# Optimization experiments

Measured on AMD Instinct MI355X. Metric: run time of the kernel, lower is better.

The kernel has to match this reference:

```python
import jax, jax.numpy as jnp
import numpy as np

N, E = 50000, 800000
NIN, H, C = 128, 4, 32          # per-head dim C = nout // nhead
ED = 44                          # edge_dim = (nin-16)/4 + 16
HC = H * C


def setup_inputs() -> dict:
    key = jax.random.key(0)
    ks = jax.random.split(key, 12)
    s = 0.05
    return {
        "x": jax.random.normal(ks[0], (N, NIN), jnp.float32),
        "edge_index": jax.random.randint(ks[1], (2, E), 0, N, jnp.int64),
        "edge_attr": jax.random.normal(ks[2], (E, ED), jnp.float32),
        "Wq": jax.random.normal(ks[3], (NIN, HC), jnp.float32) * s,
        "bq": jnp.zeros((HC,), jnp.float32),
        "Wk": jax.random.normal(ks[4], (NIN, HC), jnp.float32) * s,
        "bk": jnp.zeros((HC,), jnp.float32),
        "Wv": jax.random.normal(ks[5], (NIN, HC), jnp.float32) * s,
        "bv": jnp.zeros((HC,), jnp.float32),
        "We": jax.random.normal(ks[6], (ED, HC), jnp.float32) * s,  # lin_edge has no bias in PyG
        "Wskip": jax.random.normal(ks[7], (NIN, HC), jnp.float32) * s,
        "bskip": jnp.zeros((HC,), jnp.float32),
    }


def reference(x, edge_index, edge_attr, Wq, bq, Wk, bk, Wv, bv, We, Wskip, bskip):
    src, dst = edge_index[0], edge_index[1]  # messages flow src -> dst
    q = (x @ Wq + bq).reshape(N, H, C)
    k = (x @ Wk + bk).reshape(N, H, C)
    v = (x @ Wv + bv).reshape(N, H, C)
    e = (edge_attr @ We).reshape(E, H, C)

    k_j = k[src] + e                         # [E, H, C]
    v_j = v[src] + e                         # [E, H, C]
    alpha = jnp.einsum('ehc,ehc->eh', q[dst], k_j) / jnp.sqrt(jnp.float32(C))

    # segment softmax over incoming edges of each destination node
    m = jax.ops.segment_max(alpha, dst, num_segments=N)          # [N, H]
    a = jnp.exp(alpha - m[dst])
    denom = jax.ops.segment_sum(a, dst, num_segments=N)          # [N, H]
    a = a / (denom[dst] + 1e-16)

    agg = jax.ops.segment_sum(v_j * a[:, :, None], dst, num_segments=N)  # [N, H, C]
    out = agg.reshape(N, HC) + (x @ Wskip + bskip)               # concat heads + root skip
    return out
```

## Files before the change

### kernel.cpp

```cpp
#include <hip/hip_runtime.h>

#define N_      50000
#define E_      800000
#define HC_     128
#define ED_     44
#define NH_     4
#define DEGCAP_ 96

__global__ __launch_bounds__(256) void k_lin(
    const float* __restrict__ x,
    const float* __restrict__ Wq, const float* __restrict__ bq,
    const float* __restrict__ Wk, const float* __restrict__ bk,
    const float* __restrict__ Wv, const float* __restrict__ bv,
    const float* __restrict__ Wsk, const float* __restrict__ bsk,
    float* __restrict__ q, float* __restrict__ k, float* __restrict__ v,
    float* __restrict__ skip)
{
    __shared__ float xs[32 * 128];
    const int n0 = blockIdx.x * 32;
    const int t  = threadIdx.x;

    #pragma unroll
    for (int i = 0; i < 4; ++i) {
        int idx = t + i * 256;
        int row = idx >> 5;
        float4 a = make_float4(0.f, 0.f, 0.f, 0.f);
        if (n0 + row < N_) a = ((const float4*)x)[(size_t)n0 * 32 + idx];
        *(float4*)&xs[idx * 4] = a;
    }
    __syncthreads();

    const float* Wm[4] = {Wq, Wk, Wv, Wsk};
    const float* bm[4] = {bq, bk, bv, bsk};
    float* om[4] = {q, k, v, skip};
    const int mat = blockIdx.y;
    const float* W = Wm[mat];

    const int tx = t & 31, ty = t >> 5;
    float acc[4][4];
    #pragma unroll
    for (int r = 0; r < 4; ++r) {
        acc[r][0] = 0.f; acc[r][1] = 0.f; acc[r][2] = 0.f; acc[r][3] = 0.f;
    }

    float4 wb[4];
    #pragma unroll
    for (int dd = 0; dd < 4; ++dd)
        wb[dd] = *(const float4*)(W + dd * 128 + tx * 4);

    for (int s = 0; s < 32; ++s) {
        int sn = (s + 1) & 31;
        float4 wn[4];
        #pragma unroll
        for (int dd = 0; dd < 4; ++dd)
            wn[dd] = *(const float4*)(W + (sn * 4 + dd) * 128 + tx * 4);
        #pragma unroll
        for (int r = 0; r < 4; ++r) {
            float4 xv = *(const float4*)&xs[(ty * 4 + r) * 128 + s * 4];
            acc[r][0] += xv.x * wb[0].x + xv.y * wb[1].x + xv.z * wb[2].x + xv.w * wb[3].x;
            acc[r][1] += xv.x * wb[0].y + xv.y * wb[1].y + xv.z * wb[2].y + xv.w * wb[3].y;
            acc[r][2] += xv.x * wb[0].z + xv.y * wb[1].z + xv.z * wb[2].z + xv.w * wb[3].z;
            acc[r][3] += xv.x * wb[0].w + xv.y * wb[1].w + xv.z * wb[2].w + xv.w * wb[3].w;
        }
        #pragma unroll
        for (int dd = 0; dd < 4; ++dd) wb[dd] = wn[dd];
    }

    float4 b4 = *(const float4*)(bm[mat] + tx * 4);
    float* o = om[mat];
    #pragma unroll
    for (int r = 0; r < 4; ++r) {
        int n = n0 + ty * 4 + r;
        if (n < N_) {
            float4 rr = make_float4(acc[r][0] + b4.x, acc[r][1] + b4.y,
                                    acc[r][2] + b4.z, acc[r][3] + b4.w);
            ((float4*)(o + (size_t)n * 128))[tx] = rr;
        }
    }
}

__global__ __launch_bounds__(256) void k_scatter(const int* __restrict__ ei,
                                                 int* __restrict__ cnt,
                                                 int2* __restrict__ csr) {
    int e = blockIdx.x * 256 + threadIdx.x;
    int src = ei[e], dst = ei[E_ + e];
    int pos = atomicAdd(&cnt[dst], 1);
    if (pos < DEGCAP_) csr[(size_t)dst * DEGCAP_ + pos] = make_int2(src, e);
}

__global__ __launch_bounds__(256) void k_node(
    const int* __restrict__ cnt, const int2* __restrict__ csr,
    const float* __restrict__ ea, const float* __restrict__ We,
    const float* __restrict__ q, const float* __restrict__ k,
    const float* __restrict__ v, const float* __restrict__ skip,
    float* __restrict__ out)
{
    __shared__ float sq [4][128];
    __shared__ float sqw[4][176];
    __shared__ float srd[4][324];
    const int t = threadIdx.x, w = t >> 6, l = t & 63;
    const int n = blockIdx.x * 4 + w;

    float2 q2 = ((const float2*)(q + (size_t)n * HC_))[l];
    ((float2*)&sq[w][0])[l] = q2;

    {
        const int h = l >> 4, i16 = l & 15;
        const int d0 = 3 * i16;
        const int de0 = (d0     < ED_) ? d0     : ED_ - 1;
        const int de1 = (d0 + 1 < ED_) ? d0 + 1 : ED_ - 1;
        const int de2 = (d0 + 2 < ED_) ? d0 + 2 : ED_ - 1;
        const float* qh  = &sq[w][h * 32];
        const float* w0p = We + de0 * HC_ + h * 32;
        const float* w1p = We + de1 * HC_ + h * 32;
        const float* w2p = We + de2 * HC_ + h * 32;
        float qw0 = 0.f, qw1 = 0.f, qw2 = 0.f;
        #pragma unroll
        for (int i = 0; i < 8; ++i) {
            float4 q4 = *(const float4*)(qh  + i * 4);
            float4 a0 = *(const float4*)(w0p + i * 4);
            float4 a1 = *(const float4*)(w1p + i * 4);
            float4 a2 = *(const float4*)(w2p + i * 4);
            qw0 += q4.x*a0.x + q4.y*a0.y + q4.z*a0.z + q4.w*a0.w;
            qw1 += q4.x*a1.x + q4.y*a1.y + q4.z*a1.z + q4.w*a1.w;
            qw2 += q4.x*a2.x + q4.y*a2.y + q4.z*a2.z + q4.w*a2.w;
        }
        if (d0     < ED_) sqw[w][h * ED_ + d0]     = qw0;
        if (d0 + 1 < ED_) sqw[w][h * ED_ + d0 + 1] = qw1;
        if (d0 + 2 < ED_) sqw[w][h * ED_ + d0 + 2] = qw2;
    }

    const int g = l >> 4, ii = l & 15, eh = ii >> 2, si = ii & 3;
    const float4 qa = *(const float4*)&sq[w][eh * 32 + si * 8];
    const float4 qb = *(const float4*)&sq[w][eh * 32 + si * 8 + 4];
    float4 w0, w1, w2;
    {
        const float* wp = &sqw[w][eh * ED_ + si * 12];
        w0 = *(const float4*)wp;
        w1 = *(const float4*)(wp + 4);
        w2 = (si < 3) ? *(const float4*)(wp + 8) : make_float4(0.f,0.f,0.f,0.f);
    }
    const int eoff2 = (si < 3) ? si * 12 + 8 : 36;

    int deg = cnt[n];
    deg = deg < DEGCAP_ ? deg : DEGCAP_;
    const int2* crow = csr + (size_t)n * DEGCAP_;
    int2 c0 = make_int2(0, 0);
    if (deg > 0) c0 = crow[l < deg ? l : deg - 1];

    float4 av0 = make_float4(0.f,0.f,0.f,0.f), av1 = make_float4(0.f,0.f,0.f,0.f);
    float4 aeA = make_float4(0.f,0.f,0.f,0.f), aeB = make_float4(0.f,0.f,0.f,0.f);
    float4 aeC = make_float4(0.f,0.f,0.f,0.f);
    float ssum = 0.f;

    const int lim = deg < 64 ? deg : 64;
    for (int base = 0; base < lim; base += 8) {
        const int slotA = base + g,     slotB = base + 4 + g;
        const int scA = slotA < lim ? slotA : lim - 1;
        const int scB = slotB < lim ? slotB : lim - 1;
        const int sA = __shfl(c0.x, scA), eEA = __shfl(c0.y, scA);
        const int sB = __shfl(c0.x, scB), eEB = __shfl(c0.y, scB);

        const float* kpA = k + (size_t)sA * HC_ + eh * 32 + si * 8;
        const float* vpA = v + (size_t)sA * HC_ + eh * 32 + si * 8;
        const float* epA = ea + (size_t)eEA * ED_;
        const float* kpB = k + (size_t)sB * HC_ + eh * 32 + si * 8;
        const float* vpB = v + (size_t)sB * HC_ + eh * 32 + si * 8;
        const float* epB = ea + (size_t)eEB * ED_;
        const float4 kaA = *(const float4*)kpA;
        const float4 kbA = *(const float4*)(kpA + 4);
        const float4 vaA = *(const float4*)vpA;
        const float4 vbA = *(const float4*)(vpA + 4);
        const float4 e0A = *(const float4*)(epA + si * 12);
        const float4 e1A = *(const float4*)(epA + si * 12 + 4);
        const float4 e2A = *(const float4*)(epA + eoff2);
        const float4 kaB = *(const float4*)kpB;
        const float4 kbB = *(const float4*)(kpB + 4);
        const float4 vaB = *(const float4*)vpB;
        const float4 vbB = *(const float4*)(vpB + 4);
        const float4 e0B = *(const float4*)(epB + si * 12);
        const float4 e1B = *(const float4*)(epB + si * 12 + 4);
        const float4 e2B = *(const float4*)(epB + eoff2);

        float pA = qa.x*kaA.x + qa.y*kaA.y + qa.z*kaA.z + qa.w*kaA.w
                 + qb.x*kbA.x + qb.y*kbA.y + qb.z*kbA.z + qb.w*kbA.w
                 + w0.x*e0A.x + w0.y*e0A.y + w0.z*e0A.z + w0.w*e0A.w
                 + w1.x*e1A.x + w1.y*e1A.y + w1.z*e1A.z + w1.w*e1A.w
                 + w2.x*e2A.x + w2.y*e2A.y + w2.z*e2A.z + w2.w*e2A.w;
        float pB = qa.x*kaB.x + qa.y*kaB.y + qa.z*kaB.z + qa.w*kaB.w
                 + qb.x*kbB.x + qb.y*kbB.y + qb.z*kbB.z + qb.w*kbB.w
                 + w0.x*e0B.x + w0.y*e0B.y + w0.z*e0B.z + w0.w*e0B.w
                 + w1.x*e1B.x + w1.y*e1B.y + w1.z*e1B.z + w1.w*e1B.w
                 + w2.x*e2B.x + w2.y*e2B.y + w2.z*e2B.z + w2.w*e2B.w;
        pA += __shfl_xor(pA, 1);  pB += __shfl_xor(pB, 1);
        pA += __shfl_xor(pA, 2);  pB += __shfl_xor(pB, 2);
        const float alA = fminf(pA * 0.17677669529663687f, 40.f);
        const float alB = fminf(pB * 0.17677669529663687f, 40.f);
        const float wjA = (slotA < lim) ? __expf(alA) : 0.f;
        const float wjB = (slotB < lim) ? __expf(alB) : 0.f;

        ssum  += wjA + wjB;
        av0.x += wjA * vaA.x + wjB * vaB.x;  av0.y += wjA * vaA.y + wjB * vaB.y;
        av0.z += wjA * vaA.z + wjB * vaB.z;  av0.w += wjA * vaA.w + wjB * vaB.w;
        av1.x += wjA * vbA.x + wjB * vbB.x;  av1.y += wjA * vbA.y + wjB * vbB.y;
        av1.z += wjA * vbA.z + wjB * vbB.z;  av1.w += wjA * vbA.w + wjB * vbB.w;
        aeA.x += wjA * e0A.x + wjB * e0B.x;  aeA.y += wjA * e0A.y + wjB * e0B.y;
        aeA.z += wjA * e0A.z + wjB * e0B.z;  aeA.w += wjA * e0A.w + wjB * e0B.w;
        aeB.x += wjA * e1A.x + wjB * e1B.x;  aeB.y += wjA * e1A.y + wjB * e1B.y;
        aeB.z += wjA * e1A.z + wjB * e1B.z;  aeB.w += wjA * e1A.w + wjB * e1B.w;
        aeC.x += wjA * e2A.x + wjB * e2B.x;  aeC.y += wjA * e2A.y + wjB * e2B.y;
        aeC.z += wjA * e2A.z + wjB * e2B.z;  aeC.w += wjA * e2A.w + wjB * e2B.w;
    }

    for (int j = 64; j < deg; ++j) {
        int2 se = crow[j];
        int sA = __builtin_amdgcn_readfirstlane(se.x);
        int eA = __builtin_amdgcn_readfirstlane(se.y);
        const float* kp = k + (size_t)sA * HC_ + eh * 32 + si * 8;
        const float* vp = v + (size_t)sA * HC_ + eh * 32 + si * 8;
        const float* ep = ea + (size_t)eA * ED_;
        float4 ka = *(const float4*)kp, kb = *(const float4*)(kp + 4);
        float4 va = *(const float4*)vp, vb = *(const float4*)(vp + 4);
        float4 e0 = *(const float4*)(ep + si * 12);
        float4 e1 = *(const float4*)(ep + si * 12 + 4);
        float4 e2 = *(const float4*)(ep + eoff2);
        float p = qa.x*ka.x + qa.y*ka.y + qa.z*ka.z + qa.w*ka.w
                + qb.x*kb.x + qb.y*kb.y + qb.z*kb.z + qb.w*kb.w
                + w0.x*e0.x + w0.y*e0.y + w0.z*e0.z + w0.w*e0.w
                + w1.x*e1.x + w1.y*e1.y + w1.z*e1.z + w1.w*e1.w
                + w2.x*e2.x + w2.y*e2.y + w2.z*e2.z + w2.w*e2.w;
        p += __shfl_xor(p, 1);
        p += __shfl_xor(p, 2);
        float wj = (g == 0) ? __expf(fminf(p * 0.17677669529663687f, 40.f)) : 0.f;
        ssum  += wj;
        av0.x += wj * va.x; av0.y += wj * va.y; av0.z += wj * va.z; av0.w += wj * va.w;
        av1.x += wj * vb.x; av1.y += wj * vb.y; av1.z += wj * vb.z; av1.w += wj * vb.w;
        aeA.x += wj * e0.x; aeA.y += wj * e0.y; aeA.z += wj * e0.z; aeA.w += wj * e0.w;
        aeB.x += wj * e1.x; aeB.y += wj * e1.y; aeB.z += wj * e1.z; aeB.w += wj * e1.w;
        aeC.x += wj * e2.x; aeC.y += wj * e2.y; aeC.z += wj * e2.z; aeC.w += wj * e2.w;
    }

    #pragma unroll
    for (int d = 16; d <= 32; d <<= 1) {
        ssum  += __shfl_xor(ssum,  d);
        av0.x += __shfl_xor(av0.x, d); av0.y += __shfl_xor(av0.y, d);
        av0.z += __shfl_xor(av0.z, d); av0.w += __shfl_xor(av0.w, d);
        av1.x += __shfl_xor(av1.x, d); av1.y += __shfl_xor(av1.y, d);
        av1.z += __shfl_xor(av1.z, d); av1.w += __shfl_xor(av1.w, d);
        aeA.x += __shfl_xor(aeA.x, d); aeA.y += __shfl_xor(aeA.y, d);
        aeA.z += __shfl_xor(aeA.z, d); aeA.w += __shfl_xor(aeA.w, d);
        aeB.x += __shfl_xor(aeB.x, d); aeB.y += __shfl_xor(aeB.y, d);
        aeB.z += __shfl_xor(aeB.z, d); aeB.w += __shfl_xor(aeB.w, d);
        aeC.x += __shfl_xor(aeC.x, d); aeC.y += __shfl_xor(aeC.y, d);
        aeC.z += __shfl_xor(aeC.z, d); aeC.w += __shfl_xor(aeC.w, d);
    }

    float* sav = &srd[w][0];
    float* sae = &srd[w][128];
    float* ssm = &srd[w][320];
    if (g == 0) {
        *(float4*)&sav[eh * 32 + si * 8]     = av0;
        *(float4*)&sav[eh * 32 + si * 8 + 4] = av1;
        *(float4*)&sae[eh * 48 + si * 12]     = aeA;
        *(float4*)&sae[eh * 48 + si * 12 + 4] = aeB;
        if (si < 3) *(float4*)&sae[eh * 48 + si * 12 + 8] = aeC;
        if (si == 0) ssm[eh] = ssum;
    }

    const int h2 = l >> 4;
    float2 acc = *(const float2*)&sav[2 * l];
    float evx = 0.f, evy = 0.f;
    for (int d = 0; d < ED_; ++d) {
        float aw = sae[h2 * 48 + d];
        float2 wd = ((const float2*)(We + d * HC_))[l];
        evx += aw * wd.x;
        evy += aw * wd.y;
    }
    float inv = 1.0f / (ssm[h2] + 1e-16f);
    float2 sk = ((const float2*)(skip + (size_t)n * HC_))[l];
    ((float2*)(out + (size_t)n * HC_))[l] =
        make_float2((acc.x + evx) * inv + sk.x, (acc.y + evy) * inv + sk.y);
}

extern "C" void kernel_launch(void* const* d_in, const int* in_sizes, int n_in,
                              void* d_out, int out_size, void* d_ws, size_t ws_size,
                              hipStream_t stream)
{
    const float* x   = (const float*)d_in[0];
    const int*   ei  = (const int*)d_in[1];
    const float* ea  = (const float*)d_in[2];
    const float* Wq  = (const float*)d_in[3];
    const float* bq  = (const float*)d_in[4];
    const float* Wk  = (const float*)d_in[5];
    const float* bk  = (const float*)d_in[6];
    const float* Wv  = (const float*)d_in[7];
    const float* bv  = (const float*)d_in[8];
    const float* We  = (const float*)d_in[9];
    const float* Wsk = (const float*)d_in[10];
    const float* bsk = (const float*)d_in[11];
    float* out = (float*)d_out;

    float* ws    = (float*)d_ws;
    float* q     = ws;
    float* k     = q     + (size_t)N_ * HC_;
    float* v     = k     + (size_t)N_ * HC_;
    float* skip  = v     + (size_t)N_ * HC_;
    int*   cnt   = (int*)(skip + (size_t)N_ * HC_);
    int2*  csr   = (int2*)(cnt + N_);

    hipMemsetAsync(cnt, 0, N_ * sizeof(int), stream);
    k_lin    <<<dim3((N_ + 31) / 32, 4), 256, 0, stream>>>(
        x, Wq, bq, Wk, bk, Wv, bv, Wsk, bsk, q, k, v, skip);
    k_scatter<<<E_ / 256, 256, 0, stream>>>(ei, cnt, csr);
    k_node   <<<N_ / 4, 256, 0, stream>>>(cnt, csr, ea, We, q, k, v,
                                          skip, out);
}
```

Measured before the change: 702.1 us.

## Split node aggregation into 8-edge chunks with atomic partial accumulation

Instead of one wavefront per destination node walking all incoming edges, a new pass builds a list of (node, chunk) work items of eight edges each, and each wavefront handles one chunk. Partial softmax numerators, weighted edge sums and denominators are atomically added into global buffers, and a separate finalize kernel applies the We projection, normalization and skip. The CSR now stores only edge ids, with the source read from edge_index. This aims to balance load across skewed degrees and raise occupancy. The cost is many global float atomics, an extra zeroed workspace of about 300 floats per node, two more launches, and a q·We recomputation per chunk rather than per node.

```diff
diff --git a/kernel.cpp b/kernel.cpp
--- a/kernel.cpp
+++ b/kernel.cpp
@@ -6,6 +6,8 @@
 #define ED_     44
 #define NH_     4
 #define DEGCAP_ 96
+#define CHK_    8
+#define LCAP_   (E_ / CHK_ + N_)
 
 __global__ __launch_bounds__(256) void k_lin(
     const float* __restrict__ x,
@@ -81,25 +83,42 @@
 
 __global__ __launch_bounds__(256) void k_scatter(const int* __restrict__ ei,
                                                  int* __restrict__ cnt,
-                                                 int2* __restrict__ csr) {
+                                                 int* __restrict__ csr) {
     int e = blockIdx.x * 256 + threadIdx.x;
-    int src = ei[e], dst = ei[E_ + e];
+    int dst = ei[E_ + e];
     int pos = atomicAdd(&cnt[dst], 1);
-    if (pos < DEGCAP_) csr[(size_t)dst * DEGCAP_ + pos] = make_int2(src, e);
-}
-
-__global__ __launch_bounds__(256) void k_node(
-    const int* __restrict__ cnt, const int2* __restrict__ csr,
-    const float* __restrict__ ea, const float* __restrict__ We,
-    const float* __restrict__ q, const float* __restrict__ k,
-    const float* __restrict__ v, const float* __restrict__ skip,
-    float* __restrict__ out)
+    if (pos < DEGCAP_) csr[(size_t)dst * DEGCAP_ + pos] = e;
+}
+
+__global__ __launch_bounds__(256) void k_chunks(const int* __restrict__ cnt,
+                                                int* __restrict__ chcnt,
+                                                int* __restrict__ chlist) {
+    int n = blockIdx.x * 256 + threadIdx.x;
+    if (n >= N_) return;
+    int deg = cnt[n];
+    deg = deg < DEGCAP_ ? deg : DEGCAP_;
+    int nc = (deg + CHK_ - 1) / CHK_;
+    if (nc == 0) return;
+    int pos = atomicAdd(chcnt, nc);
+    for (int j = 0; j < nc; ++j) chlist[pos + j] = (n << 4) | j;
+}
+
+__global__ __launch_bounds__(512) void k_node(
+    const int* __restrict__ chcnt, const int* __restrict__ chlist,
+    const int* __restrict__ cnt, const int* __restrict__ csr,
+    const int* __restrict__ ei, const float* __restrict__ ea,
+    const float* __restrict__ We, const float* __restrict__ q,
+    const float* __restrict__ k, const float* __restrict__ v,
+    float* __restrict__ sav, float* __restrict__ sae,
+    float* __restrict__ sbuf)
 {
-    __shared__ float sq [4][128];
-    __shared__ float sqw[4][176];
-    __shared__ float srd[4][324];
+    __shared__ float sq [8][128];
+    __shared__ float sqw[8][176];
     const int t = threadIdx.x, w = t >> 6, l = t & 63;
-    const int n = blockIdx.x * 4 + w;
+    const int id = blockIdx.x * 8 + w;
+    if (id >= chcnt[0]) return;
+    const int p = chlist[id];
+    const int n = p >> 4, c = p & 15;
 
     float2 q2 = ((const float2*)(q + (size_t)n * HC_))[l];
     ((float2*)&sq[w][0])[l] = q2;
@@ -144,101 +163,67 @@
 
     int deg = cnt[n];
     deg = deg < DEGCAP_ ? deg : DEGCAP_;
-    const int2* crow = csr + (size_t)n * DEGCAP_;
-    int2 c0 = make_int2(0, 0);
-    if (deg > 0) c0 = crow[l < deg ? l : deg - 1];
-
-    float4 av0 = make_float4(0.f,0.f,0.f,0.f), av1 = make_float4(0.f,0.f,0.f,0.f);
-    float4 aeA = make_float4(0.f,0.f,0.f,0.f), aeB = make_float4(0.f,0.f,0.f,0.f);
-    float4 aeC = make_float4(0.f,0.f,0.f,0.f);
-    float ssum = 0.f;
-
-    const int lim = deg < 64 ? deg : 64;
-    for (int base = 0; base < lim; base += 8) {
-        const int slotA = base + g,     slotB = base + 4 + g;
-        const int scA = slotA < lim ? slotA : lim - 1;
-        const int scB = slotB < lim ? slotB : lim - 1;
-        const int sA = __shfl(c0.x, scA), eEA = __shfl(c0.y, scA);
-        const int sB = __shfl(c0.x, scB), eEB = __shfl(c0.y, scB);
-
-        const float* kpA = k + (size_t)sA * HC_ + eh * 32 + si * 8;
-        const float* vpA = v + (size_t)sA * HC_ + eh * 32 + si * 8;
-        const float* epA = ea + (size_t)eEA * ED_;
-        const float* kpB = k + (size_t)sB * HC_ + eh * 32 + si * 8;
-        const float* vpB = v + (size_t)sB * HC_ + eh * 32 + si * 8;
-        const float* epB = ea + (size_t)eEB * ED_;
-        const float4 kaA = *(const float4*)kpA;
-        const float4 kbA = *(const float4*)(kpA + 4);
-        const float4 vaA = *(const float4*)vpA;
-        const float4 vbA = *(const float4*)(vpA + 4);
-        const float4 e0A = *(const float4*)(epA + si * 12);
-        const float4 e1A = *(const float4*)(epA + si * 12 + 4);
-        const float4 e2A = *(const float4*)(epA + eoff2);
-        const float4 kaB = *(const float4*)kpB;
-        const float4 kbB = *(const float4*)(kpB + 4);
-        const float4 vaB = *(const float4*)vpB;
-        const float4 vbB = *(const float4*)(vpB + 4);
-        const float4 e0B = *(const float4*)(epB + si * 12);
-        const float4 e1B = *(const float4*)(epB + si * 12 + 4);
-        const float4 e2B = *(const float4*)(epB + eoff2);
-
-        float pA = qa.x*kaA.x + qa.y*kaA.y + qa.z*kaA.z + qa.w*kaA.w
-                 + qb.x*kbA.x + qb.y*kbA.y + qb.z*kbA.z + qb.w*kbA.w
-                 + w0.x*e0A.x + w0.y*e0A.y + w0.z*e0A.z + w0.w*e0A.w
-                 + w1.x*e1A.x + w1.y*e1A.y + w1.z*e1A.z + w1.w*e1A.w
-                 + w2.x*e2A.x + w2.y*e2A.y + w2.z*e2A.z + w2.w*e2A.w;
-        float pB = qa.x*kaB.x + qa.y*kaB.y + qa.z*kaB.z + qa.w*kaB.w
-                 + qb.x*kbB.x + qb.y*kbB.y + qb.z*kbB.z + qb.w*kbB.w
-                 + w0.x*e0B.x + w0.y*e0B.y + w0.z*e0B.z + w0.w*e0B.w
-                 + w1.x*e1B.x + w1.y*e1B.y + w1.z*e1B.z + w1.w*e1B.w
-                 + w2.x*e2B.x + w2.y*e2B.y + w2.z*e2B.z + w2.w*e2B.w;
-        pA += __shfl_xor(pA, 1);  pB += __shfl_xor(pB, 1);
-        pA += __shfl_xor(pA, 2);  pB += __shfl_xor(pB, 2);
-        const float alA = fminf(pA * 0.17677669529663687f, 40.f);
-        const float alB = fminf(pB * 0.17677669529663687f, 40.f);
-        const float wjA = (slotA < lim) ? __expf(alA) : 0.f;
-        const float wjB = (slotB < lim) ? __expf(alB) : 0.f;
-
-        ssum  += wjA + wjB;
-        av0.x += wjA * vaA.x + wjB * vaB.x;  av0.y += wjA * vaA.y + wjB * vaB.y;
-        av0.z += wjA * vaA.z + wjB * vaB.z;  av0.w += wjA * vaA.w + wjB * vaB.w;
-        av1.x += wjA * vbA.x + wjB * vbB.x;  av1.y += wjA * vbA.y + wjB * vbB.y;
-        av1.z += wjA * vbA.z + wjB * vbB.z;  av1.w += wjA * vbA.w + wjB * vbB.w;
-        aeA.x += wjA * e0A.x + wjB * e0B.x;  aeA.y += wjA * e0A.y + wjB * e0B.y;
-        aeA.z += wjA * e0A.z + wjB * e0B.z;  aeA.w += wjA * e0A.w + wjB * e0B.w;
-        aeB.x += wjA * e1A.x + wjB * e1B.x;  aeB.y += wjA * e1A.y + wjB * e1B.y;
-        aeB.z += wjA * e1A.z + wjB * e1B.z;  aeB.w += wjA * e1A.w + wjB * e1B.w;
-        aeC.x += wjA * e2A.x + wjB * e2B.x;  aeC.y += wjA * e2A.y + wjB * e2B.y;
-        aeC.z += wjA * e2A.z + wjB * e2B.z;  aeC.w += wjA * e2A.w + wjB * e2B.w;
-    }
-
-    for (int j = 64; j < deg; ++j) {
-        int2 se = crow[j];
-        int sA = __builtin_amdgcn_readfirstlane(se.x);
-        int eA = __builtin_amdgcn_readfirstlane(se.y);
-        const float* kp = k + (size_t)sA * HC_ + eh * 32 + si * 8;
-        const float* vp = v + (size_t)sA * HC_ + eh * 32 + si * 8;
-        const float* ep = ea + (size_t)eA * ED_;
-        float4 ka = *(const float4*)kp, kb = *(const float4*)(kp + 4);
-        float4 va = *(const float4*)vp, vb = *(const float4*)(vp + 4);
-        float4 e0 = *(const float4*)(ep + si * 12);
-        float4 e1 = *(const float4*)(ep + si * 12 + 4);
-        float4 e2 = *(const float4*)(ep + eoff2);
-        float p = qa.x*ka.x + qa.y*ka.y + qa.z*ka.z + qa.w*ka.w
-                + qb.x*kb.x + qb.y*kb.y + qb.z*kb.z + qb.w*kb.w
-                + w0.x*e0.x + w0.y*e0.y + w0.z*e0.z + w0.w*e0.w
-                + w1.x*e1.x + w1.y*e1.y + w1.z*e1.z + w1.w*e1.w
-                + w2.x*e2.x + w2.y*e2.y + w2.z*e2.z + w2.w*e2.w;
-        p += __shfl_xor(p, 1);
-        p += __shfl_xor(p, 2);
-        float wj = (g == 0) ? __expf(fminf(p * 0.17677669529663687f, 40.f)) : 0.f;
-        ssum  += wj;
-        av0.x += wj * va.x; av0.y += wj * va.y; av0.z += wj * va.z; av0.w += wj * va.w;
-        av1.x += wj * vb.x; av1.y += wj * vb.y; av1.z += wj * vb.z; av1.w += wj * vb.w;
-        aeA.x += wj * e0.x; aeA.y += wj * e0.y; aeA.z += wj * e0.z; aeA.w += wj * e0.w;
-        aeB.x += wj * e1.x; aeB.y += wj * e1.y; aeB.z += wj * e1.z; aeB.w += wj * e1.w;
-        aeC.x += wj * e2.x; aeC.y += wj * e2.y; aeC.z += wj * e2.z; aeC.w += wj * e2.w;
-    }
+    const int rem = deg - c * CHK_;
+
+    int idx = c * CHK_ + (l & 7);
+    if (idx >= deg) idx = deg - 1;
+    const int eId  = csr[(size_t)n * DEGCAP_ + idx];
+    const int srcN = ei[eId];
+
+    const int slotA = g, slotB = 4 + g;
+    const int sA = __shfl(srcN, slotA), eEA = __shfl(eId, slotA);
+    const int sB = __shfl(srcN, slotB), eEB = __shfl(eId, slotB);
+
+    const float* kpA = k + (size_t)sA * HC_ + eh * 32 + si * 8;
+    const float* vpA = v + (size_t)sA * HC_ + eh * 32 + si * 8;
+    const float* epA = ea + (size_t)eEA * ED_;
+    const float* kpB = k + (size_t)sB * HC_ + eh * 32 + si * 8;
+    const float* vpB = v + (size_t)sB * HC_ + eh * 32 + si * 8;
+    const float* epB = ea + (size_t)eEB * ED_;
+    const float4 kaA = *(const float4*)kpA;
+    const float4 kbA = *(const float4*)(kpA + 4);
+    const float4 vaA = *(const float4*)vpA;
+    const float4 vbA = *(const float4*)(vpA + 4);
+    const float4 e0A = *(const float4*)(epA + si * 12);
+    const float4 e1A = *(const float4*)(epA + si * 12 + 4);
+    const float4 e2A = *(const float4*)(epA + eoff2);
+    const float4 kaB = *(const float4*)kpB;
+    const float4 kbB = *(const float4*)(kpB + 4);
+    const float4 vaB = *(const float4*)vpB;
+    const float4 vbB = *(const float4*)(vpB + 4);
+    const float4 e0B = *(const float4*)(epB + si * 12);
+    const float4 e1B = *(const float4*)(epB + si * 12 + 4);
+    const float4 e2B = *(const float4*)(epB + eoff2);
+
+    float pA = qa.x*kaA.x + qa.y*kaA.y + qa.z*kaA.z + qa.w*kaA.w
+             + qb.x*kbA.x + qb.y*kbA.y + qb.z*kbA.z + qb.w*kbA.w
+             + w0.x*e0A.x + w0.y*e0A.y + w0.z*e0A.z + w0.w*e0A.w
+             + w1.x*e1A.x + w1.y*e1A.y + w1.z*e1A.z + w1.w*e1A.w
+             + w2.x*e2A.x + w2.y*e2A.y + w2.z*e2A.z + w2.w*e2A.w;
+    float pB = qa.x*kaB.x + qa.y*kaB.y + qa.z*kaB.z + qa.w*kaB.w
+             + qb.x*kbB.x + qb.y*kbB.y + qb.z*kbB.z + qb.w*kbB.w
+             + w0.x*e0B.x + w0.y*e0B.y + w0.z*e0B.z + w0.w*e0B.w
+             + w1.x*e1B.x + w1.y*e1B.y + w1.z*e1B.z + w1.w*e1B.w
+             + w2.x*e2B.x + w2.y*e2B.y + w2.z*e2B.z + w2.w*e2B.w;
+    pA += __shfl_xor(pA, 1);  pB += __shfl_xor(pB, 1);
+    pA += __shfl_xor(pA, 2);  pB += __shfl_xor(pB, 2);
+    const float alA = fminf(pA * 0.17677669529663687f, 40.f);
+    const float alB = fminf(pB * 0.17677669529663687f, 40.f);
+    const float wjA = (slotA < rem) ? __expf(alA) : 0.f;
+    const float wjB = (slotB < rem) ? __expf(alB) : 0.f;
+
+    float ssum = wjA + wjB;
+    float4 av0, av1, aeA, aeB, aeC;
+    av0.x = wjA * vaA.x + wjB * vaB.x;  av0.y = wjA * vaA.y + wjB * vaB.y;
+    av0.z = wjA * vaA.z + wjB * vaB.z;  av0.w = wjA * vaA.w + wjB * vaB.w;
+    av1.x = wjA * vbA.x + wjB * vbB.x;  av1.y = wjA * vbA.y + wjB * vbB.y;
+    av1.z = wjA * vbA.z + wjB * vbB.z;  av1.w = wjA * vbA.w + wjB * vbB.w;
+    aeA.x = wjA * e0A.x + wjB * e0B.x;  aeA.y = wjA * e0A.y + wjB * e0B.y;
+    aeA.z = wjA * e0A.z + wjB * e0B.z;  aeA.w = wjA * e0A.w + wjB * e0B.w;
+    aeB.x = wjA * e1A.x + wjB * e1B.x;  aeB.y = wjA * e1A.y + wjB * e1B.y;
+    aeB.z = wjA * e1A.z + wjB * e1B.z;  aeB.w = wjA * e1A.w + wjB * e1B.w;
+    aeC.x = wjA * e2A.x + wjB * e2B.x;  aeC.y = wjA * e2A.y + wjB * e2B.y;
+    aeC.z = wjA * e2A.z + wjB * e2B.z;  aeC.w = wjA * e2A.w + wjB * e2B.w;
 
     #pragma unroll
     for (int d = 16; d <= 32; d <<= 1) {
@@ -255,28 +240,44 @@
         aeC.z += __shfl_xor(aeC.z, d); aeC.w += __shfl_xor(aeC.w, d);
     }
 
-    float* sav = &srd[w][0];
-    float* sae = &srd[w][128];
-    float* ssm = &srd[w][320];
     if (g == 0) {
-        *(float4*)&sav[eh * 32 + si * 8]     = av0;
-        *(float4*)&sav[eh * 32 + si * 8 + 4] = av1;
-        *(float4*)&sae[eh * 48 + si * 12]     = aeA;
-        *(float4*)&sae[eh * 48 + si * 12 + 4] = aeB;
-        if (si < 3) *(float4*)&sae[eh * 48 + si * 12 + 8] = aeC;
-        if (si == 0) ssm[eh] = ssum;
-    }
-
+        float* pv = sav + (size_t)n * HC_ + eh * 32 + si * 8;
+        atomicAdd(pv + 0, av0.x); atomicAdd(pv + 1, av0.y);
+        atomicAdd(pv + 2, av0.z); atomicAdd(pv + 3, av0.w);
+        atomicAdd(pv + 4, av1.x); atomicAdd(pv + 5, av1.y);
+        atomicAdd(pv + 6, av1.z); atomicAdd(pv + 7, av1.w);
+        float* pe = sae + (size_t)n * 176 + eh * 44 + si * 12;
+        atomicAdd(pe + 0, aeA.x); atomicAdd(pe + 1, aeA.y);
+        atomicAdd(pe + 2, aeA.z); atomicAdd(pe + 3, aeA.w);
+        atomicAdd(pe + 4, aeB.x); atomicAdd(pe + 5, aeB.y);
+        atomicAdd(pe + 6, aeB.z); atomicAdd(pe + 7, aeB.w);
+        if (si < 3) {
+            atomicAdd(pe + 8,  aeC.x); atomicAdd(pe + 9,  aeC.y);
+            atomicAdd(pe + 10, aeC.z); atomicAdd(pe + 11, aeC.w);
+        }
+        if (si == 0) atomicAdd(sbuf + (size_t)n * 4 + eh, ssum);
+    }
+}
+
+__global__ __launch_bounds__(512) void k_fin(
+    const float* __restrict__ sav, const float* __restrict__ sae,
+    const float* __restrict__ sbuf, const float* __restrict__ We,
+    const float* __restrict__ skip, float* __restrict__ out)
+{
+    const int t = threadIdx.x, w = t >> 6, l = t & 63;
+    const int n = blockIdx.x * 8 + w;
+    if (n >= N_) return;
     const int h2 = l >> 4;
-    float2 acc = *(const float2*)&sav[2 * l];
+    float2 acc = ((const float2*)(sav + (size_t)n * HC_))[l];
+    const float* ae = sae + (size_t)n * 176 + h2 * 44;
     float evx = 0.f, evy = 0.f;
     for (int d = 0; d < ED_; ++d) {
-        float aw = sae[h2 * 48 + d];
+        float aw = ae[d];
         float2 wd = ((const float2*)(We + d * HC_))[l];
         evx += aw * wd.x;
         evy += aw * wd.y;
     }
-    float inv = 1.0f / (ssm[h2] + 1e-16f);
+    float inv = 1.0f / (sbuf[(size_t)n * 4 + h2] + 1e-16f);
     float2 sk = ((const float2*)(skip + (size_t)n * HC_))[l];
     ((float2*)(out + (size_t)n * HC_))[l] =
         make_float2((acc.x + evx) * inv + sk.x, (acc.y + evy) * inv + sk.y);
@@ -300,18 +301,26 @@
     const float* bsk = (const float*)d_in[11];
     float* out = (float*)d_out;
 
-    float* ws    = (float*)d_ws;
-    float* q     = ws;
-    float* k     = q     + (size_t)N_ * HC_;
-    float* v     = k     + (size_t)N_ * HC_;
-    float* skip  = v     + (size_t)N_ * HC_;
-    int*   cnt   = (int*)(skip + (size_t)N_ * HC_);
-    int2*  csr   = (int2*)(cnt + N_);
-
-    hipMemsetAsync(cnt, 0, N_ * sizeof(int), stream);
+    float* ws     = (float*)d_ws;
+    float* q      = ws;
+    float* k      = q    + (size_t)N_ * HC_;
+    float* v      = k    + (size_t)N_ * HC_;
+    float* skip   = v    + (size_t)N_ * HC_;
+    float* sav    = skip + (size_t)N_ * HC_;
+    float* sae    = sav  + (size_t)N_ * HC_;
+    float* sbuf   = sae  + (size_t)N_ * 176;
+    int*   cnt    = (int*)(sbuf + (size_t)N_ * 4);
+    int*   chcnt  = cnt + N_;
+    int*   chlist = chcnt + 1;
+    int*   csr    = chlist + LCAP_;
+
+    hipMemsetAsync(cnt, 0, (N_ + 1) * sizeof(int), stream);
+    hipMemsetAsync(sav, 0, (size_t)N_ * (HC_ + 176 + 4) * sizeof(float), stream);
     k_lin    <<<dim3((N_ + 31) / 32, 4), 256, 0, stream>>>(
         x, Wq, bq, Wk, bk, Wv, bv, Wsk, bsk, q, k, v, skip);
     k_scatter<<<E_ / 256, 256, 0, stream>>>(ei, cnt, csr);
-    k_node   <<<N_ / 4, 256, 0, stream>>>(cnt, csr, ea, We, q, k, v,
-                                          skip, out);
-}
+    k_chunks <<<(N_ + 255) / 256, 256, 0, stream>>>(cnt, chcnt, chlist);
+    k_node   <<<LCAP_ / 8, 512, 0, stream>>>(chcnt, chlist, cnt, csr, ei, ea,
+                                             We, q, k, v, sav, sae, sbuf);
+    k_fin    <<<(N_ + 7) / 8, 512, 0, stream>>>(sav, sae, sbuf, We, skip, out);
+}
```

Measured after the change: 2.077 ms. 2.96x slower.

## Fuse four projection GEMMs into one pass per node row without shared-memory tiling

Applied to the files above, without the earlier changes.

The linear kernel now handles all four weight matrices (q, k, v, skip) in one launch. Each warp-row computes one node, reading x directly from global memory instead of staging a 32-row tile in shared memory. This removes the extra grid dimension and re-reads of x across four matrix launches. In exchange, each block covers only 8 nodes, so weight rows are re-read from cache far more often and per-thread register reuse of x across rows is lost.

```diff
diff --git a/kernel.cpp b/kernel.cpp
--- a/kernel.cpp
+++ b/kernel.cpp
@@ -16,67 +16,51 @@
     float* __restrict__ q, float* __restrict__ k, float* __restrict__ v,
     float* __restrict__ skip)
 {
-    __shared__ float xs[32 * 128];
-    const int n0 = blockIdx.x * 32;
-    const int t  = threadIdx.x;
-
-    #pragma unroll
-    for (int i = 0; i < 4; ++i) {
-        int idx = t + i * 256;
-        int row = idx >> 5;
-        float4 a = make_float4(0.f, 0.f, 0.f, 0.f);
-        if (n0 + row < N_) a = ((const float4*)x)[(size_t)n0 * 32 + idx];
-        *(float4*)&xs[idx * 4] = a;
-    }
-    __syncthreads();
-
-    const float* Wm[4] = {Wq, Wk, Wv, Wsk};
-    const float* bm[4] = {bq, bk, bv, bsk};
-    float* om[4] = {q, k, v, skip};
-    const int mat = blockIdx.y;
-    const float* W = Wm[mat];
-
-    const int tx = t & 31, ty = t >> 5;
-    float acc[4][4];
-    #pragma unroll
-    for (int r = 0; r < 4; ++r) {
-        acc[r][0] = 0.f; acc[r][1] = 0.f; acc[r][2] = 0.f; acc[r][3] = 0.f;
-    }
-
-    float4 wb[4];
-    #pragma unroll
-    for (int dd = 0; dd < 4; ++dd)
-        wb[dd] = *(const float4*)(W + dd * 128 + tx * 4);
-
-    for (int s = 0; s < 32; ++s) {
-        int sn = (s + 1) & 31;
-        float4 wn[4];
+    const int t = threadIdx.x;
+    const int r = t >> 5, c = t & 31;
+    const int n = blockIdx.x * 8 + r;
+
+    const float4* x4  = (const float4*)(x + (size_t)n * HC_);
+    const float4* Wq4 = (const float4*)Wq;
+    const float4* Wk4 = (const float4*)Wk;
+    const float4* Wv4 = (const float4*)Wv;
+    const float4* Ws4 = (const float4*)Wsk;
+
+    float4 aq = make_float4(0.f, 0.f, 0.f, 0.f);
+    float4 ak = make_float4(0.f, 0.f, 0.f, 0.f);
+    float4 av = make_float4(0.f, 0.f, 0.f, 0.f);
+    float4 as = make_float4(0.f, 0.f, 0.f, 0.f);
+
+    #pragma unroll 4
+    for (int d4 = 0; d4 < 32; ++d4) {
+        const float4 xv = x4[d4];
         #pragma unroll
-        for (int dd = 0; dd < 4; ++dd)
-            wn[dd] = *(const float4*)(W + (sn * 4 + dd) * 128 + tx * 4);
-        #pragma unroll
-        for (int r = 0; r < 4; ++r) {
-            float4 xv = *(const float4*)&xs[(ty * 4 + r) * 128 + s * 4];
-            acc[r][0] += xv.x * wb[0].x + xv.y * wb[1].x + xv.z * wb[2].x + xv.w * wb[3].x;
-            acc[r][1] += xv.x * wb[0].y + xv.y * wb[1].y + xv.z * wb[2].y + xv.w * wb[3].y;
-            acc[r][2] += xv.x * wb[0].z + xv.y * wb[1].z + xv.z * wb[2].z + xv.w * wb[3].z;
-            acc[r][3] += xv.x * wb[0].w + xv.y * wb[1].w + xv.z * wb[2].w + xv.w * wb[3].w;
+        for (int dd = 0; dd < 4; ++dd) {
+            const float xs = dd == 0 ? xv.x : dd == 1 ? xv.y : dd == 2 ? xv.z : xv.w;
+            const int wi = (d4 * 4 + dd) * 32 + c;
+            const float4 wq = Wq4[wi];
+            const float4 wk = Wk4[wi];
+            const float4 wv = Wv4[wi];
+            const float4 ws = Ws4[wi];
+            aq.x += xs * wq.x; aq.y += xs * wq.y; aq.z += xs * wq.z; aq.w += xs * wq.w;
+            ak.x += xs * wk.x; ak.y += xs * wk.y; ak.z += xs * wk.z; ak.w += xs * wk.w;
+            av.x += xs * wv.x; av.y += xs * wv.y; av.z += xs * wv.z; av.w += xs * wv.w;
+            as.x += xs * ws.x; as.y += xs * ws.y; as.z += xs * ws.z; as.w += xs * ws.w;
         }
-        #pragma unroll
-        for (int dd = 0; dd < 4; ++dd) wb[dd] = wn[dd];
-    }
-
-    float4 b4 = *(const float4*)(bm[mat] + tx * 4);
-    float* o = om[mat];
-    #pragma unroll
-    for (int r = 0; r < 4; ++r) {
-        int n = n0 + ty * 4 + r;
-        if (n < N_) {
-            float4 rr = make_float4(acc[r][0] + b4.x, acc[r][1] + b4.y,
-                                    acc[r][2] + b4.z, acc[r][3] + b4.w);
-            ((float4*)(o + (size_t)n * 128))[tx] = rr;
-        }
-    }
+    }
+
+    const float4 b0 = ((const float4*)bq)[c];
+    const float4 b1 = ((const float4*)bk)[c];
+    const float4 b2 = ((const float4*)bv)[c];
+    const float4 b3 = ((const float4*)bsk)[c];
+    ((float4*)(q    + (size_t)n * HC_))[c] =
+        make_float4(aq.x + b0.x, aq.y + b0.y, aq.z + b0.z, aq.w + b0.w);
+    ((float4*)(k    + (size_t)n * HC_))[c] =
+        make_float4(ak.x + b1.x, ak.y + b1.y, ak.z + b1.z, ak.w + b1.w);
+    ((float4*)(v    + (size_t)n * HC_))[c] =
+        make_float4(av.x + b2.x, av.y + b2.y, av.z + b2.z, av.w + b2.w);
+    ((float4*)(skip + (size_t)n * HC_))[c] =
+        make_float4(as.x + b3.x, as.y + b3.y, as.z + b3.z, as.w + b3.w);
 }
 
 __global__ __launch_bounds__(256) void k_scatter(const int* __restrict__ ei,
@@ -309,8 +293,8 @@
     int2*  csr   = (int2*)(cnt + N_);
 
     hipMemsetAsync(cnt, 0, N_ * sizeof(int), stream);
-    k_lin    <<<dim3((N_ + 31) / 32, 4), 256, 0, stream>>>(
-        x, Wq, bq, Wk, bk, Wv, bv, Wsk, bsk, q, k, v, skip);
+    k_lin    <<<N_ / 8, 256, 0, stream>>>(x, Wq, bq, Wk, bk, Wv, bv,
+                                          Wsk, bsk, q, k, v, skip);
     k_scatter<<<E_ / 256, 256, 0, stream>>>(ei, cnt, csr);
     k_node   <<<N_ / 4, 256, 0, stream>>>(cnt, csr, ea, We, q, k, v,
                                           skip, out);
```

Result: slower. 1.003 ms (+42.8%).
